# Kernel tuning notes

Measured on AMD Instinct MI355X. Metric: run time of the kernel, lower is better.

## Reference

```python
import jax, jax.numpy as jnp
import numpy as np
from jax import lax

B, S, C_IN, D, H, P, W, DFF, K = 32, 4096, 32, 256, 8, 24, 64, 512, 5
DH = D // H
EPS = 1e-5


def _make_starts():
    stride = max(1, W // 2)
    idx = list(range(0, max(S - W + 1, 1), stride))
    if len(idx) == 0 or idx[-1] != S - W:
        if S - W >= 0:
            idx.append(S - W)
    return np.asarray(idx)

STARTS = _make_starts()                      # [M]
WIDX = STARTS[:, None] + np.arange(W)        # [M, W] patch gather indices


def setup_inputs() -> dict:
    key = jax.random.key(0)
    ks = jax.random.split(key, 24)
    r = lambda i, shape, s=0.02: (jax.random.normal(ks[i], shape, jnp.float32) * s)
    return {
        "x": jax.random.normal(ks[0], (B, S, C_IN), jnp.float32),
        "last_close_unused": jnp.zeros((B,), jnp.float32),
        "dw_w": r(1, (C_IN, 1, K), 0.2),      # depthwise conv kernel
        "pw_w": r(2, (D, C_IN), 0.1),         # pointwise conv (1x1)
        "bn_g": jnp.ones((D,), jnp.float32),
        "bn_b": jnp.zeros((D,), jnp.float32),
        "lg_Wq": r(3, (D, D)), "lg_Wk": r(4, (D, D)),
        "lg_Wv": r(5, (D, D)), "lg_Wo": r(6, (D, D)),
        "dec_Qd": r(7, (P, D), 1.0 / np.sqrt(D)),
        "dec_Wq": r(8, (D, D)), "dec_Wk": r(9, (D, D)),
        "dec_Wv": r(10, (D, D)), "dec_Wo": r(11, (D, D)),
        "ff1_w": r(12, (DFF, D)), "ff1_b": jnp.zeros((DFF,), jnp.float32),
        "ff2_w": r(13, (D, DFF)), "ff2_b": jnp.zeros((D,), jnp.float32),
        "out_w": r(14, (1, D)), "out_b": jnp.zeros((1,), jnp.float32),
        "gate_logits": jnp.tile(jnp.array([0.2, 0.4, 0.4], jnp.float32), (P, 1)),
    }


def _ln(x):
    m = x.mean(-1, keepdims=True)
    v = ((x - m) ** 2).mean(-1, keepdims=True)
    return (x - m) / jnp.sqrt(v + EPS)


def _split(t):  # [B, L, D] -> [B, H, L, DH]
    return t.reshape(t.shape[0], -1, H, DH).transpose(0, 2, 1, 3)


def _mha(Q, KV, Wq, Wk, Wv, scale):
    q = _split(Q @ Wq.T)
    k = _split(KV @ Wk.T)
    v = _split(KV @ Wv.T)
    attn = jax.nn.softmax(jnp.einsum('bhqd,bhkd->bhqk', q, k) * scale, axis=-1)
    o = jnp.einsum('bhqk,bhkd->bhqd', attn, v)
    o = o.transpose(0, 2, 1, 3).reshape(Q.shape[0], -1, D)
    return o, attn


def reference(x, last_close_unused, dw_w, pw_w, bn_g, bn_b,
              lg_Wq, lg_Wk, lg_Wv, lg_Wo,
              dec_Qd, dec_Wq, dec_Wk, dec_Wv, dec_Wo,
              ff1_w, ff1_b, ff2_w, ff2_b, out_w, out_b, gate_logits):
    # --- DepthwisePointwise front-end ---
    xt = jnp.transpose(x, (0, 2, 1))                         # [B, C, S]
    z = lax.conv_general_dilated(xt, dw_w, (1,), [(K // 2, K // 2)],
                                 dimension_numbers=('NCH', 'OIH', 'NCH'),
                                 feature_group_count=C_IN)
    z = jnp.einsum('dc,bcs->bds', pw_w, z)                   # pointwise 1x1
    z = jax.nn.gelu(z, approximate=False)
    m = z.mean((0, 2), keepdims=True)                        # BatchNorm1d (batch stats)
    v = ((z - m) ** 2).mean((0, 2), keepdims=True)
    z = (z - m) / jnp.sqrt(v + EPS) * bn_g[None, :, None] + bn_b[None, :, None]
    z = jnp.transpose(z, (0, 2, 1))                          # [B, S, D]

    # --- LocalGlobalAttention: patch-mean queries over full sequence K/V ---
    Q = z[:, WIDX].mean(axis=2)                              # [B, M, D]
    scale = 1.0 / np.sqrt(DH)
    o, attn_g = _mha(Q, z, lg_Wq, lg_Wk, lg_Wv, scale)
    Hh = _ln(o @ lg_Wo.T + Q)                                # [B, M, D]

    # --- CrossDecoder: learned queries ---
    Qd = jnp.broadcast_to(dec_Qd[None], (B, P, D))
    o2, attn_d = _mha(Qd, Hh, dec_Wq, dec_Wk, dec_Wv, scale)
    z2 = _ln(o2 @ dec_Wo.T + Qd)
    u = jax.nn.gelu(z2 @ ff1_w.T + ff1_b, approximate=False)
    u = _ln(u @ ff2_w.T + ff2_b + z2)
    y_global = (u @ out_w.T + out_b)[..., 0]                 # [B, P]

    # --- Gated combine: residual=0, local=global ---
    g = jax.nn.softmax(gate_logits, axis=-1)                 # [P, 3]
    y = g[:, 1][None, :] * y_global + g[:, 2][None, :] * y_global
    return (y, attn_g, attn_d)
```

## Files before the change

### kernel.cpp

```cpp
#include <hip/hip_runtime.h>
#include <hip/hip_bf16.h>
#include <cmath>

typedef unsigned short u16;
typedef __attribute__((ext_vector_type(4))) float f32x4;
typedef __attribute__((ext_vector_type(8))) short s16x8;

__device__ __forceinline__ float b2f(u16 u) { return __uint_as_float(((unsigned)u) << 16); }
__device__ __forceinline__ u16 f2b(float f) {
    unsigned u = __float_as_uint(f);
    unsigned r = (u + 0x7fffu + ((u >> 16) & 1u)) >> 16;
    return (u16)r;
}
__device__ __forceinline__ float gelu_f(float x) {
    return 0.5f * x * (1.0f + erff(x * 0.70710678118654752f));
}

#define FOLD 0.25503590f

__global__ __launch_bounds__(256) void prep0_k(const float* __restrict__ pw_w,
        const float* __restrict__ lg_Wq, const float* __restrict__ lg_Wo,
        const float* __restrict__ dec_Wk, const float* __restrict__ dec_Wv,
        const float* __restrict__ dec_Wo, const float* __restrict__ ff1_w,
        const float* __restrict__ ff2_w,
        u16* __restrict__ pwb, u16* __restrict__ Wq_b, u16* __restrict__ Wo_b,
        u16* __restrict__ Wk2_b, u16* __restrict__ Wv2_b, u16* __restrict__ Wo2b,
        u16* __restrict__ ff1b, u16* __restrict__ ff2b)
{
    int idx = blockIdx.x * 256 + threadIdx.x;
    if (idx < 327680) {
        int which = idx >> 16, r = idx & 65535;
        const float* srcs[5] = {lg_Wq, lg_Wo, dec_Wk, dec_Wv, dec_Wo};
        u16* dsts[5] = {Wq_b, Wo_b, Wk2_b, Wv2_b, Wo2b};
        dsts[which][r] = f2b(srcs[which][r]);
    } else if (idx < 458752) {
        int r = idx - 327680;
        ff1b[r] = f2b(ff1_w[r]);
    } else if (idx < 589824) {
        int r = idx - 458752;
        ff2b[r] = f2b(ff2_w[r]);
    } else {
        int r = idx - 589824;
        pwb[r] = f2b(pw_w[r]);
    }
}

__global__ __launch_bounds__(256) void dwpw_k(const float* __restrict__ x,
        const float* __restrict__ dw_w, const u16* __restrict__ pwb,
        u16* __restrict__ zp, float* __restrict__ csum, float* __restrict__ csum2)
{
    __shared__ float xs[68][33];
    __shared__ __align__(16) u16 As[64][40];
    const int t = threadIdx.x;
    const int b = blockIdx.x >> 6, s0 = (blockIdx.x & 63) << 6;
    const int r0 = blockIdx.x * 64;
    const int lane = t & 63, w = t >> 6;
    const int l16 = lane & 15, hi = lane >> 4;

    for (int idx = t; idx < 68 * 32; idx += 256) {
        int row = idx >> 5, c = idx & 31;
        int sg = s0 - 2 + row;
        xs[row][c] = (sg >= 0 && sg < 4096) ? x[((size_t)b * 4096 + sg) * 32 + c] : 0.0f;
    }
    const int cc = t & 31;
    float wv[5];
    #pragma unroll
    for (int k = 0; k < 5; ++k) wv[k] = dw_w[cc * 5 + k];
    __syncthreads();
    #pragma unroll
    for (int i = 0; i < 8; ++i) {
        int sl = (t + i * 256) >> 5;
        float acc = 0;
        #pragma unroll
        for (int k = 0; k < 5; ++k) acc += xs[sl + k][cc] * wv[k];
        As[sl][cc] = f2b(acc);
    }
    __syncthreads();

    const int n0 = w * 64;
    f32x4 zero = {0, 0, 0, 0};
    s16x8 bf[4];
    #pragma unroll
    for (int ni = 0; ni < 4; ++ni)
        bf[ni] = *(const s16x8*)(pwb + (n0 + ni * 16 + l16) * 32 + hi * 8);

    float cl[4] = {0,0,0,0}, ch[4] = {0,0,0,0};
    float ql[4] = {0,0,0,0}, qh[4] = {0,0,0,0};

    #pragma unroll
    for (int mi = 0; mi < 4; ++mi) {
        s16x8 af = *(const s16x8*)&As[mi * 16 + l16][hi * 8];
        #pragma unroll
        for (int ni = 0; ni < 4; ++ni) {
            f32x4 acc = __builtin_amdgcn_mfma_f32_16x16x32_bf16(af, bf[ni], zero, 0, 0, 0);
            int col = n0 + ni * 16 + l16;
            int rowb = r0 + mi * 16 + hi * 4;
            #pragma unroll
            for (int r = 0; r < 4; ++r) {
                float e = gelu_f(acc[r]);
                zp[(size_t)(rowb + r) * 256 + col] = f2b(e);
                if (mi < 2) { cl[ni] += e; ql[ni] += e * e; }
                else        { ch[ni] += e; qh[ni] += e * e; }
            }
        }
    }
    #pragma unroll
    for (int ni = 0; ni < 4; ++ni) {
        #pragma unroll
        for (int m = 16; m <= 32; m <<= 1) {
            cl[ni] += __shfl_xor(cl[ni], m);
            ch[ni] += __shfl_xor(ch[ni], m);
            ql[ni] += __shfl_xor(ql[ni], m);
            qh[ni] += __shfl_xor(qh[ni], m);
        }
        if (lane < 16) {
            int col = n0 + ni * 16 + lane;
            size_t bc = (size_t)(r0 >> 5);
            csum [bc * 256 + col]       = cl[ni];
            csum [(bc + 1) * 256 + col] = ch[ni];
            csum2[bc * 256 + col]       = ql[ni];
            csum2[(bc + 1) * 256 + col] = qh[ni];
        }
    }
}

__global__ __launch_bounds__(256) void stats2_k(const float* __restrict__ csum,
        const float* __restrict__ csum2, float* __restrict__ statp)
{
    int j = blockIdx.x, t = threadIdx.x;
    float s1 = 0, s2 = 0;
    for (int i = 0; i < 64; ++i) {
        s1 += csum [(size_t)(j * 64 + i) * 256 + t];
        s2 += csum2[(size_t)(j * 64 + i) * 256 + t];
    }
    statp[j * 512 + t] = s1;
    statp[j * 512 + 256 + t] = s2;
}

__global__ __launch_bounds__(256) void prep1_k(const float* __restrict__ statp,
        const float* __restrict__ bn_g, const float* __restrict__ bn_b,
        const float* __restrict__ gate_logits,
        float* __restrict__ a_ws, float* __restrict__ c_ws, float* __restrict__ coef)
{
    int t = threadIdx.x;
    float s1 = 0, s2 = 0;
    for (int j = 0; j < 64; ++j) {
        s1 += statp[j * 512 + t];
        s2 += statp[j * 512 + 256 + t];
    }
    const float invN = 1.0f / 131072.0f;
    float mean = s1 * invN;
    float var = s2 * invN - mean * mean;
    float av = bn_g[t] * rsqrtf(var + 1e-5f);
    a_ws[t] = av;
    c_ws[t] = bn_b[t] - mean * av;
    if (t < 24) {
        float g0 = gate_logits[t * 3], g1 = gate_logits[t * 3 + 1], g2 = gate_logits[t * 3 + 2];
        float mx = fmaxf(g0, fmaxf(g1, g2));
        float e0 = __expf(g0 - mx), e1 = __expf(g1 - mx), e2 = __expf(g2 - mx);
        coef[t] = (e1 + e2) / (e0 + e1 + e2);
    }
}

__global__ __launch_bounds__(256) void prep2b_k(const float* __restrict__ lg_Wk,
        const float* __restrict__ lg_Wv, const float* __restrict__ a_ws,
        const float* __restrict__ c_ws,
        u16* __restrict__ Wk_b, u16* __restrict__ Wv_b,
        float* __restrict__ betak, float* __restrict__ betav)
{
    __shared__ float red[4];
    int bid = blockIdx.x;
    int which = bid >> 8, row = bid & 255, t = threadIdx.x;
    const float* Wsrc = which ? lg_Wv : lg_Wk;
    float wv = Wsrc[row * 256 + t];
    (which ? Wv_b : Wk_b)[row * 256 + t] = f2b(wv * a_ws[t]);
    float v = wv * c_ws[t];
    for (int m = 32; m; m >>= 1) v += __shfl_xor(v, m);
    if ((t & 63) == 0) red[t >> 6] = v;
    __syncthreads();
    if (t == 0) (which ? betav : betak)[row] = red[0] + red[1] + red[2] + red[3];
}

__global__ __launch_bounds__(256) void q2_k(const float* __restrict__ dec_Qd,
        const float* __restrict__ dec_Wq, float* __restrict__ q2)
{
    __shared__ float wq[16][260];
    __shared__ float qd[24][260];
    int j = blockIdx.x, t = threadIdx.x;
    for (int idx = t; idx < 4096; idx += 256) {
        int tl = idx >> 8, d = idx & 255;
        wq[tl][d] = dec_Wq[(j * 16 + tl) * 256 + d];
    }
    for (int idx = t; idx < 6144; idx += 256) {
        int p = idx >> 8, d = idx & 255;
        qd[p][d] = dec_Qd[idx];
    }
    __syncthreads();
    for (int o = t; o < 384; o += 256) {
        int p = o >> 4, tl = o & 15;
        float s = 0;
        #pragma unroll 8
        for (int d = 0; d < 256; ++d) s += qd[p][d] * wq[tl][d];
        q2[p * 256 + j * 16 + tl] = s;
    }
}

__global__ __launch_bounds__(256) void qgemm_k(const float* __restrict__ csum,
        const float* __restrict__ a_ws, const float* __restrict__ c_ws,
        const u16* __restrict__ W, u16* __restrict__ qb)
{
    __shared__ u16 As[64 * 256];
    __shared__ float aa[256], ccx[256];
    const int t = threadIdx.x;
    const int r0 = blockIdx.x * 64;
    const int lane = t & 63, w = t >> 6;
    const int l16 = lane & 15, hi = lane >> 4;

    aa[t] = a_ws[t] * 0.015625f;
    ccx[t] = c_ws[t];
    __syncthreads();

    #pragma unroll
    for (int i = 0; i < 8; ++i) {
        int c = t + i * 256;
        int row = c >> 5, c16 = c & 31;
        int g = r0 + row, mm = g & 127;
        u16 tmp[8];
        if (mm == 127) {
            #pragma unroll
            for (int j = 0; j < 8; ++j) tmp[j] = 0;
        } else {
            const float* c0p = csum + (size_t)g * 256 + c16 * 8;
            const float* c1p = c0p + 256;
            #pragma unroll
            for (int j = 0; j < 8; ++j) {
                int d = c16 * 8 + j;
                tmp[j] = f2b((c0p[j] + c1p[j]) * aa[d] + ccx[d]);
            }
        }
        int boff = (c16 * 16) ^ ((row & 7) << 4);
        *(s16x8*)((char*)As + row * 512 + boff) = *(s16x8*)tmp;
    }
    __syncthreads();

    const int n0 = w * 64;
    f32x4 zero = {0, 0, 0, 0};
    f32x4 acc[4][4];
    #pragma unroll
    for (int mi = 0; mi < 4; ++mi)
        #pragma unroll
        for (int ni = 0; ni < 4; ++ni) acc[mi][ni] = zero;

    #pragma unroll
    for (int kk = 0; kk < 8; ++kk) {
        s16x8 af[4], bf[4];
        #pragma unroll
        for (int mi = 0; mi < 4; ++mi) {
            int row = mi * 16 + l16;
            int boff = (kk * 64 + hi * 16) ^ ((row & 7) << 4);
            af[mi] = *(const s16x8*)((const char*)As + row * 512 + boff);
        }
        #pragma unroll
        for (int ni = 0; ni < 4; ++ni)
            bf[ni] = *(const s16x8*)(W + (n0 + ni * 16 + l16) * 256 + kk * 32 + hi * 8);
        #pragma unroll
        for (int mi = 0; mi < 4; ++mi)
            #pragma unroll
            for (int ni = 0; ni < 4; ++ni)
                acc[mi][ni] = __builtin_amdgcn_mfma_f32_16x16x32_bf16(af[mi], bf[ni], acc[mi][ni], 0, 0, 0);
    }

    #pragma unroll
    for (int mi = 0; mi < 4; ++mi)
        #pragma unroll
        for (int ni = 0; ni < 4; ++ni) {
            int col = n0 + ni * 16 + l16;
            int rowb = r0 + mi * 16 + hi * 4;
            #pragma unroll
            for (int r = 0; r < 4; ++r)
                qb[(size_t)(rowb + r) * 256 + col] = f2b(acc[mi][ni][r] * FOLD);
        }
}

__global__ __launch_bounds__(256) void kv_k(const u16* __restrict__ zp,
        const u16* __restrict__ Wk, const u16* __restrict__ Wv,
        const float* __restrict__ betak, const float* __restrict__ betav,
        u16* __restrict__ kb, u16* __restrict__ vT)
{
    __shared__ u16 As[64 * 256];
    const int t = threadIdx.x;
    const int r0 = blockIdx.x * 64;
    const int lane = t & 63, w = t >> 6;
    const int l16 = lane & 15, hi = lane >> 4;

    const u16* Ag = zp + (size_t)r0 * 256;
    #pragma unroll
    for (int i = 0; i < 8; ++i) {
        int c = t + i * 256;
        int row = c >> 5, c16 = c & 31;
        s16x8 v = *(const s16x8*)(Ag + row * 256 + c16 * 8);
        int boff = (c16 * 16) ^ ((row & 7) << 4);
        *(s16x8*)((char*)As + row * 512 + boff) = v;
    }
    __syncthreads();

    const int n0 = w * 64;
    f32x4 zero = {0, 0, 0, 0};
    f32x4 acc[4][4];
    #pragma unroll
    for (int mi = 0; mi < 4; ++mi)
        #pragma unroll
        for (int ni = 0; ni < 4; ++ni) acc[mi][ni] = zero;

    #pragma unroll
    for (int kk = 0; kk < 8; ++kk) {
        s16x8 af[4], bfk[4];
        #pragma unroll
        for (int mi = 0; mi < 4; ++mi) {
            int row = mi * 16 + l16;
            int boff = (kk * 64 + hi * 16) ^ ((row & 7) << 4);
            af[mi] = *(const s16x8*)((const char*)As + row * 512 + boff);
        }
        #pragma unroll
        for (int ni = 0; ni < 4; ++ni)
            bfk[ni] = *(const s16x8*)(Wk + (n0 + ni * 16 + l16) * 256 + kk * 32 + hi * 8);
        #pragma unroll
        for (int mi = 0; mi < 4; ++mi)
            #pragma unroll
            for (int ni = 0; ni < 4; ++ni)
                acc[mi][ni] = __builtin_amdgcn_mfma_f32_16x16x32_bf16(af[mi], bfk[ni], acc[mi][ni], 0, 0, 0);
    }
    #pragma unroll
    for (int mi = 0; mi < 4; ++mi)
        #pragma unroll
        for (int ni = 0; ni < 4; ++ni) {
            int col = n0 + ni * 16 + l16;
            float bv = betak[col];
            int rowb = r0 + mi * 16 + hi * 4;
            #pragma unroll
            for (int r = 0; r < 4; ++r)
                kb[(size_t)(rowb + r) * 256 + col] = f2b(acc[mi][ni][r] + bv);
        }

    #pragma unroll
    for (int mi = 0; mi < 4; ++mi)
        #pragma unroll
        for (int ni = 0; ni < 4; ++ni) acc[mi][ni] = zero;
    #pragma unroll
    for (int kk = 0; kk < 8; ++kk) {
        s16x8 af[4], bfv[4];
        #pragma unroll
        for (int mi = 0; mi < 4; ++mi) {
            int row = mi * 16 + l16;
            int boff = (kk * 64 + hi * 16) ^ ((row & 7) << 4);
            af[mi] = *(const s16x8*)((const char*)As + row * 512 + boff);
        }
        #pragma unroll
        for (int ni = 0; ni < 4; ++ni)
            bfv[ni] = *(const s16x8*)(Wv + (n0 + ni * 16 + l16) * 256 + kk * 32 + hi * 8);
        #pragma unroll
        for (int mi = 0; mi < 4; ++mi)
            #pragma unroll
            for (int ni = 0; ni < 4; ++ni)
                acc[mi][ni] = __builtin_amdgcn_mfma_f32_16x16x32_bf16(af[mi], bfv[ni], acc[mi][ni], 0, 0, 0);
    }
    const int b = r0 >> 12, sbase = r0 & 4095;
    #pragma unroll
    for (int mi = 0; mi < 4; ++mi)
        #pragma unroll
        for (int ni = 0; ni < 4; ++ni) {
            int col = n0 + ni * 16 + l16;
            float bv = betav[col];
            int h = col >> 5, dh = col & 31;
            int s = sbase + mi * 16 + hi * 4;
            ushort4 pk;
            pk.x = f2b(acc[mi][ni][0] + bv);
            pk.y = f2b(acc[mi][ni][1] + bv);
            pk.z = f2b(acc[mi][ni][2] + bv);
            pk.w = f2b(acc[mi][ni][3] + bv);
            *(ushort4*)(vT + ((size_t)((b * 8 + h) * 32 + dh)) * 4096 + s) = pk;
        }
}

template<int MODE>
__global__ __launch_bounds__(256) void gemm_g(const u16* __restrict__ A,
        const u16* __restrict__ W, const float* __restrict__ bias,
        void* __restrict__ Cout, int K, int ntn)
{
    __shared__ u16 As[64 * 256];
    const int t = threadIdx.x;
    const int rt = blockIdx.x / ntn, nt = blockIdx.x % ntn;
    const int r0 = rt * 64, N = ntn * 256;
    const int lane = t & 63, w = t >> 6;
    const int l16 = lane & 15, hi = lane >> 4;

    const u16* Ag = A + (size_t)r0 * K;
    const int n0 = w * 64;
    f32x4 zero = {0, 0, 0, 0};
    f32x4 acc[4][4];
    #pragma unroll
    for (int mi = 0; mi < 4; ++mi)
        #pragma unroll
        for (int ni = 0; ni < 4; ++ni) acc[mi][ni] = zero;

    for (int kc = 0; kc < K; kc += 256) {
        if (kc) __syncthreads();
        #pragma unroll
        for (int i = 0; i < 8; ++i) {
            int c = t + i * 256;
            int row = c >> 5, c16 = c & 31;
            s16x8 v = *(const s16x8*)(Ag + (size_t)row * K + kc + c16 * 8);
            int boff = (c16 * 16) ^ ((row & 7) << 4);
            *(s16x8*)((char*)As + row * 512 + boff) = v;
        }
        __syncthreads();
        #pragma unroll
        for (int kk = 0; kk < 8; ++kk) {
            s16x8 af[4], bf[4];
            #pragma unroll
            for (int mi = 0; mi < 4; ++mi) {
                int row = mi * 16 + l16;
                int boff = (kk * 64 + hi * 16) ^ ((row & 7) << 4);
                af[mi] = *(const s16x8*)((const char*)As + row * 512 + boff);
            }
            #pragma unroll
            for (int ni = 0; ni < 4; ++ni) {
                int j = nt * 256 + n0 + ni * 16 + l16;
                bf[ni] = *(const s16x8*)(W + (size_t)j * K + kc + kk * 32 + hi * 8);
            }
            #pragma unroll
            for (int mi = 0; mi < 4; ++mi)
                #pragma unroll
                for (int ni = 0; ni < 4; ++ni)
                    acc[mi][ni] = __builtin_amdgcn_mfma_f32_16x16x32_bf16(af[mi], bf[ni], acc[mi][ni], 0, 0, 0);
        }
    }

    #pragma unroll
    for (int mi = 0; mi < 4; ++mi)
        #pragma unroll
        for (int ni = 0; ni < 4; ++ni) {
            int col = nt * 256 + n0 + ni * 16 + l16;
            float bv = bias ? bias[col] : 0.0f;
            int rowb = r0 + mi * 16 + hi * 4;
            #pragma unroll
            for (int r = 0; r < 4; ++r) {
                float v = acc[mi][ni][r] + bv;
                if (MODE == 0)      ((u16*)Cout)[(size_t)(rowb + r) * N + col] = f2b(v);
                else if (MODE == 1) ((float*)Cout)[(size_t)(rowb + r) * N + col] = v;
                else                ((u16*)Cout)[(size_t)(rowb + r) * N + col] = f2b(gelu_f(v));
            }
        }
}

__global__ __launch_bounds__(256) void gemm_dual(const u16* __restrict__ A,
        const u16* __restrict__ W0, const u16* __restrict__ W1,
        u16* __restrict__ C0, u16* __restrict__ C1)
{
    __shared__ u16 As[64 * 256];
    const int t = threadIdx.x;
    const int which = blockIdx.x >> 6;
    const int r0 = (blockIdx.x & 63) * 64;
    const u16* W = which ? W1 : W0;
    u16* C = which ? C1 : C0;
    const int lane = t & 63, w = t >> 6;
    const int l16 = lane & 15, hi = lane >> 4;

    const u16* Ag = A + (size_t)r0 * 256;
    #pragma unroll
    for (int i = 0; i < 8; ++i) {
        int c = t + i * 256;
        int row = c >> 5, c16 = c & 31;
        s16x8 v = *(const s16x8*)(Ag + row * 256 + c16 * 8);
        int boff = (c16 * 16) ^ ((row & 7) << 4);
        *(s16x8*)((char*)As + row * 512 + boff) = v;
    }
    __syncthreads();

    const int n0 = w * 64;
    f32x4 zero = {0, 0, 0, 0};
    f32x4 acc[4][4];
    #pragma unroll
    for (int mi = 0; mi < 4; ++mi)
        #pragma unroll
        for (int ni = 0; ni < 4; ++ni) acc[mi][ni] = zero;

    #pragma unroll
    for (int kk = 0; kk < 8; ++kk) {
        s16x8 af[4], bf[4];
        #pragma unroll
        for (int mi = 0; mi < 4; ++mi) {
            int row = mi * 16 + l16;
            int boff = (kk * 64 + hi * 16) ^ ((row & 7) << 4);
            af[mi] = *(const s16x8*)((const char*)As + row * 512 + boff);
        }
        #pragma unroll
        for (int ni = 0; ni < 4; ++ni)
            bf[ni] = *(const s16x8*)(W + (n0 + ni * 16 + l16) * 256 + kk * 32 + hi * 8);
        #pragma unroll
        for (int mi = 0; mi < 4; ++mi)
            #pragma unroll
            for (int ni = 0; ni < 4; ++ni)
                acc[mi][ni] = __builtin_amdgcn_mfma_f32_16x16x32_bf16(af[mi], bf[ni], acc[mi][ni], 0, 0, 0);
    }
    #pragma unroll
    for (int mi = 0; mi < 4; ++mi)
        #pragma unroll
        for (int ni = 0; ni < 4; ++ni) {
            int col = n0 + ni * 16 + l16;
            int rowb = r0 + mi * 16 + hi * 4;
            #pragma unroll
            for (int r = 0; r < 4; ++r)
                C[(size_t)(rowb + r) * 256 + col] = f2b(acc[mi][ni][r]);
        }
}

__global__ __launch_bounds__(512) void attn_p1(const u16* __restrict__ qb,
        const u16* __restrict__ kb, const u16* __restrict__ vT,
        float* __restrict__ den, float* __restrict__ o_part)
{
    const int bid = blockIdx.x;
    const int b = bid >> 6, h = (bid >> 3) & 7, chunk = bid & 7;
    const int t = threadIdx.x, w = t >> 6, lane = t & 63;
    const int l16 = lane & 15, hi = lane >> 4;

    __shared__ u16 p_lds[8][16][48];

    s16x8 qf = *(const s16x8*)(qb + ((size_t)(b * 128 + w * 16 + l16)) * 256 + h * 32 + hi * 8);
    const u16* kbase = kb + (size_t)b * 4096 * 256 + h * 32 + hi * 8;
    const u16* vbase = vT + ((size_t)(b * 8 + h)) * 32 * 4096 + hi * 8;

    float dacc[4] = {0, 0, 0, 0};
    f32x4 zero = {0, 0, 0, 0};
    f32x4 oacc[2]; oacc[0] = zero; oacc[1] = zero;

    const int sbeg = chunk * 512, send = sbeg + 512;
    s16x8 kf0 = *(const s16x8*)(kbase + (size_t)(sbeg + l16) * 256);
    s16x8 kf1 = *(const s16x8*)(kbase + (size_t)(sbeg + 16 + l16) * 256);
    s16x8 vf0 = *(const s16x8*)(vbase + ((size_t)l16) * 4096 + sbeg);
    s16x8 vf1 = *(const s16x8*)(vbase + ((size_t)(16 + l16)) * 4096 + sbeg);

    for (int s0 = sbeg; s0 < send; s0 += 32) {
        s16x8 k0 = kf0, k1 = kf1, v0 = vf0, v1 = vf1;
        int sn = s0 + 32;
        if (sn < send) {
            kf0 = *(const s16x8*)(kbase + (size_t)(sn + l16) * 256);
            kf1 = *(const s16x8*)(kbase + (size_t)(sn + 16 + l16) * 256);
            vf0 = *(const s16x8*)(vbase + ((size_t)l16) * 4096 + sn);
            vf1 = *(const s16x8*)(vbase + ((size_t)(16 + l16)) * 4096 + sn);
        }
        f32x4 lg0 = __builtin_amdgcn_mfma_f32_16x16x32_bf16(qf, k0, zero, 0, 0, 0);
        f32x4 lg1 = __builtin_amdgcn_mfma_f32_16x16x32_bf16(qf, k1, zero, 0, 0, 0);
        #pragma unroll
        for (int r = 0; r < 4; ++r) {
            float e0 = exp2f(lg0[r]);
            float e1 = exp2f(lg1[r]);
            dacc[r] += e0 + e1;
            p_lds[w][hi * 4 + r][l16] = f2b(e0);
            p_lds[w][hi * 4 + r][16 + l16] = f2b(e1);
        }
        s16x8 pf = *(const s16x8*)(&p_lds[w][l16][hi * 8]);
        oacc[0] = __builtin_amdgcn_mfma_f32_16x16x32_bf16(pf, v0, oacc[0], 0, 0, 0);
        oacc[1] = __builtin_amdgcn_mfma_f32_16x16x32_bf16(pf, v1, oacc[1], 0, 0, 0);
    }

    #pragma unroll
    for (int m = 1; m <= 8; m <<= 1) {
        #pragma unroll
        for (int r = 0; r < 4; ++r) dacc[r] += __shfl_xor(dacc[r], m);
    }
    if (l16 == 0) {
        #pragma unroll
        for (int r = 0; r < 4; ++r)
            den[(size_t)chunk * 32768 + (b * 8 + h) * 128 + w * 16 + hi * 4 + r] = dacc[r];
    }
    #pragma unroll
    for (int vi = 0; vi < 2; ++vi)
        #pragma unroll
        for (int r = 0; r < 4; ++r) {
            int mg = w * 16 + hi * 4 + r;
            o_part[(size_t)chunk * 1048576 + (size_t)(b * 128 + mg) * 256 + h * 32 + vi * 16 + l16] = oacc[vi][r];
        }
}

__global__ __launch_bounds__(256) void dinv_k(const float* __restrict__ den, float* __restrict__ den_inv)
{
    int i = blockIdx.x * 256 + threadIdx.x;
    float s = 0;
    #pragma unroll
    for (int c = 0; c < 8; ++c) s += den[(size_t)c * 32768 + i];
    den_inv[i] = 1.0f / s;
}

__global__ __launch_bounds__(256) void norm_k(const float* __restrict__ o_part,
        const float* __restrict__ den_inv, u16* __restrict__ ob)
{
    size_t idx = (size_t)blockIdx.x * 256 + threadIdx.x;
    int row = (int)(idx >> 8);
    int col = (int)(idx & 255);
    int b = row >> 7, m = row & 127, h = col >> 5;
    float s = 0;
    #pragma unroll
    for (int c = 0; c < 8; ++c) s += o_part[(size_t)c * 1048576 + idx];
    ob[idx] = f2b(s * den_inv[b * 1024 + h * 128 + m]);
}

__global__ __launch_bounds__(512) void attn_p2(const u16* __restrict__ qb,
        const u16* __restrict__ kb, const float* __restrict__ den_inv,
        float* __restrict__ attn_out)
{
    const int bid = blockIdx.x;
    const int b = bid >> 6, h = (bid >> 3) & 7, chunk = bid & 7;
    const int t = threadIdx.x, w = t >> 6, lane = t & 63;
    const int l16 = lane & 15, hi = lane >> 4;

    __shared__ float buf[8][16][68];

    s16x8 qf = *(const s16x8*)(qb + ((size_t)(b * 128 + w * 16 + l16)) * 256 + h * 32 + hi * 8);
    const u16* kbase = kb + (size_t)b * 4096 * 256 + h * 32 + hi * 8;

    float rinv[4];
    #pragma unroll
    for (int r = 0; r < 4; ++r)
        rinv[r] = den_inv[b * 1024 + h * 128 + w * 16 + hi * 4 + r];

    f32x4 zero = {0, 0, 0, 0};
    float* ab = attn_out + (size_t)(b * 8 + h) * 127 * 4096;
    const int nrow = (w < 7) ? 16 : 15;

    const int sbeg = chunk * 512, send = sbeg + 512;
    for (int s0 = sbeg; s0 < send; s0 += 64) {
        #pragma unroll
        for (int kk = 0; kk < 4; ++kk) {
            int sg = s0 + kk * 16 + l16;
            s16x8 kf = *(const s16x8*)(kbase + (size_t)sg * 256);
            f32x4 lg = __builtin_amdgcn_mfma_f32_16x16x32_bf16(qf, kf, zero, 0, 0, 0);
            #pragma unroll
            for (int r = 0; r < 4; ++r)
                buf[w][hi * 4 + r][kk * 16 + l16] = exp2f(lg[r]) * rinv[r];
        }
        float* dst = ab + (size_t)(w * 16) * 4096 + s0 + lane;
        for (int r = 0; r < nrow; ++r)
            dst[(size_t)r * 4096] = buf[w][r][lane];
    }
}

__global__ __launch_bounds__(256) void ln_hh(const float* __restrict__ og,
        const float* __restrict__ csum, const float* __restrict__ a_ws,
        const float* __restrict__ c_ws, u16* __restrict__ Hb)
{
    __shared__ float red[8];
    int row = blockIdx.x, t = threadIdx.x;
    int mm = row & 127;
    float qv = 0.0f;
    if (mm != 127)
        qv = (csum[(size_t)row * 256 + t] + csum[(size_t)(row + 1) * 256 + t]) *
             (0.015625f * a_ws[t]) + c_ws[t];
    float v = og[(size_t)row * 256 + t] + qv;
    float s = v;
    for (int m = 32; m; m >>= 1) s += __shfl_xor(s, m);
    if ((t & 63) == 0) red[t >> 6] = s;
    __syncthreads();
    float mean = (red[0] + red[1] + red[2] + red[3]) * (1.0f / 256.0f);
    __syncthreads();
    float d = v - mean;
    float q = d * d;
    for (int m = 32; m; m >>= 1) q += __shfl_xor(q, m);
    if ((t & 63) == 0) red[t >> 6] = q;
    __syncthreads();
    float var = (red[0] + red[1] + red[2] + red[3]) * (1.0f / 256.0f);
    Hb[(size_t)row * 256 + t] = f2b(d * rsqrtf(var + 1e-5f));
}

__global__ __launch_bounds__(256) void dec_attn_k(const float* __restrict__ q2,
        const u16* __restrict__ k2b, const u16* __restrict__ v2b,
        float* __restrict__ attn_d, u16* __restrict__ o2b)
{
    __shared__ float qs2[24 * 32];
    __shared__ float ks[128][33];
    __shared__ float vs[128][33];
    __shared__ float lg2[24 * 128];
    __shared__ float sinv[24];
    int bid = blockIdx.x, b = bid >> 3, h = bid & 7;
    int t = threadIdx.x;
    const float scale = 0.17677669529663687f;
    for (int idx = t; idx < 4096; idx += 256) {
        int row = idx >> 5, c = idx & 31;
        ks[row][c] = b2f(k2b[((size_t)(b * 128 + row)) * 256 + h * 32 + c]);
        vs[row][c] = b2f(v2b[((size_t)(b * 128 + row)) * 256 + h * 32 + c]);
    }
    for (int idx = t; idx < 768; idx += 256) {
        int p = idx >> 5, i = idx & 31;
        qs2[idx] = q2[p * 256 + h * 32 + i];
    }
    __syncthreads();
    for (int idx = t; idx < 3048; idx += 256) {
        int p = idx / 127, m = idx - p * 127;
        float s = 0;
        #pragma unroll 8
        for (int i = 0; i < 32; ++i) s += qs2[p * 32 + i] * ks[m][i];
        lg2[p * 128 + m] = __expf(s * scale);
    }
    __syncthreads();
    if (t < 24) {
        float s = 0;
        for (int m = 0; m < 127; ++m) s += lg2[t * 128 + m];
        sinv[t] = 1.0f / s;
    }
    __syncthreads();
    float* ad = attn_d + (size_t)bid * 24 * 127;
    for (int idx = t; idx < 3048; idx += 256) {
        int p = idx / 127, m = idx - p * 127;
        float av = lg2[p * 128 + m] * sinv[p];
        lg2[p * 128 + m] = av;
        ad[idx] = av;
    }
    __syncthreads();
    for (int idx = t; idx < 768; idx += 256) {
        int p = idx >> 5, dh = idx & 31;
        float s = 0;
        for (int m = 0; m < 127; ++m)
            s += lg2[p * 128 + m] * vs[m][dh];
        o2b[((size_t)(b * 24 + p)) * 256 + h * 32 + dh] = f2b(s);
    }
}

__global__ __launch_bounds__(256) void ln3_k(const float* __restrict__ og2,
        const float* __restrict__ dec_Qd, float* __restrict__ z2f, u16* __restrict__ z2b)
{
    __shared__ float red[8];
    int row = blockIdx.x, p = row % 24, t = threadIdx.x;
    float v = og2[(size_t)row * 256 + t] + dec_Qd[p * 256 + t];
    float s = v;
    for (int m = 32; m; m >>= 1) s += __shfl_xor(s, m);
    if ((t & 63) == 0) red[t >> 6] = s;
    __syncthreads();
    float mean = (red[0] + red[1] + red[2] + red[3]) * (1.0f / 256.0f);
    __syncthreads();
    float d = v - mean, q = d * d;
    for (int m = 32; m; m >>= 1) q += __shfl_xor(q, m);
    if ((t & 63) == 0) red[t >> 6] = q;
    __syncthreads();
    float var = (red[0] + red[1] + red[2] + red[3]) * (1.0f / 256.0f);
    float u = d * rsqrtf(var + 1e-5f);
    z2f[(size_t)row * 256 + t] = u;
    z2b[(size_t)row * 256 + t] = f2b(u);
}

__global__ __launch_bounds__(256) void ln5_k(const float* __restrict__ uraw,
        const float* __restrict__ z2f, const float* __restrict__ out_w,
        const float* __restrict__ out_b, const float* __restrict__ coef,
        float* __restrict__ y)
{
    __shared__ float red[8];
    int row = blockIdx.x, p = row % 24, t = threadIdx.x;
    float v = uraw[(size_t)row * 256 + t] + z2f[(size_t)row * 256 + t];
    float s = v;
    for (int m = 32; m; m >>= 1) s += __shfl_xor(s, m);
    if ((t & 63) == 0) red[t >> 6] = s;
    __syncthreads();
    float mean = (red[0] + red[1] + red[2] + red[3]) * (1.0f / 256.0f);
    __syncthreads();
    float d = v - mean, q = d * d;
    for (int m = 32; m; m >>= 1) q += __shfl_xor(q, m);
    if ((t & 63) == 0) red[t >> 6] = q;
    __syncthreads();
    float var = (red[0] + red[1] + red[2] + red[3]) * (1.0f / 256.0f);
    float u = d * rsqrtf(var + 1e-5f);
    __syncthreads();
    float yp = u * out_w[t];
    for (int m = 32; m; m >>= 1) yp += __shfl_xor(yp, m);
    if ((t & 63) == 0) red[t >> 6] = yp;
    __syncthreads();
    if (t == 0) {
        float tot = red[0] + red[1] + red[2] + red[3] + out_b[0];
        y[row] = coef[p] * tot;
    }
}

extern "C" void kernel_launch(void* const* d_in, const int* in_sizes, int n_in,
                              void* d_out, int out_size, void* d_ws, size_t ws_size,
                              hipStream_t stream)
{
    const float* x        = (const float*)d_in[0];
    const float* dw_w     = (const float*)d_in[2];
    const float* pw_w     = (const float*)d_in[3];
    const float* bn_g     = (const float*)d_in[4];
    const float* bn_b     = (const float*)d_in[5];
    const float* lg_Wq    = (const float*)d_in[6];
    const float* lg_Wk    = (const float*)d_in[7];
    const float* lg_Wv    = (const float*)d_in[8];
    const float* lg_Wo    = (const float*)d_in[9];
    const float* dec_Qd   = (const float*)d_in[10];
    const float* dec_Wq   = (const float*)d_in[11];
    const float* dec_Wk   = (const float*)d_in[12];
    const float* dec_Wv   = (const float*)d_in[13];
    const float* dec_Wo   = (const float*)d_in[14];
    const float* ff1_w    = (const float*)d_in[15];
    const float* ff1_b    = (const float*)d_in[16];
    const float* ff2_w    = (const float*)d_in[17];
    const float* ff2_b    = (const float*)d_in[18];
    const float* out_w    = (const float*)d_in[19];
    const float* out_b    = (const float*)d_in[20];
    const float* gate_lg  = (const float*)d_in[21];

    char* ws = (char*)d_ws;
    size_t off = 0;
    auto alloc = [&](size_t bytes) -> void* {
        void* p = ws + off;
        off = (off + bytes + 255) & ~(size_t)255;
        return p;
    };
    u16*   zp    = (u16*)  alloc(67108864);
    u16*   kb    = (u16*)  alloc(67108864);
    u16*   vT    = (u16*)  alloc(67108864);
    float* csum  = (float*)alloc(4194304);
    float* csum2 = (float*)alloc(4194304);
    u16*   qb    = (u16*)  alloc(2097152);
    u16*   ob    = (u16*)  alloc(2097152);
    float* og    = (float*)alloc(4194304);
    u16*   Hb    = (u16*)  alloc(2097152);
    u16*   k2b   = (u16*)  alloc(2097152);
    u16*   v2b   = (u16*)  alloc(2097152);
    float* o_part= (float*)alloc(33554432);
    u16*   o2b   = (u16*)  alloc(393216);
    float* og2   = (float*)alloc(786432);
    float* z2f   = (float*)alloc(786432);
    u16*   z2b   = (u16*)  alloc(393216);
    u16*   u1b   = (u16*)  alloc(786432);
    float* uraw  = (float*)alloc(786432);
    float* q2    = (float*)alloc(24576);
    float* den   = (float*)alloc(1048576);
    float* den_i = (float*)alloc(131072);
    float* statp = (float*)alloc(131072);
    float* a_ws  = (float*)alloc(1024);
    float* c_ws  = (float*)alloc(1024);
    float* betak = (float*)alloc(1024);
    float* betav = (float*)alloc(1024);
    float* coef  = (float*)alloc(256);
    u16*   pwb   = (u16*)  alloc(16384);
    u16*   Wk_b  = (u16*)  alloc(131072);
    u16*   Wv_b  = (u16*)  alloc(131072);
    u16*   Wq_b  = (u16*)  alloc(131072);
    u16*   Wo_b  = (u16*)  alloc(131072);
    u16*   Wk2_b = (u16*)  alloc(131072);
    u16*   Wv2_b = (u16*)  alloc(131072);
    u16*   Wo2b  = (u16*)  alloc(131072);
    u16*   ff1b  = (u16*)  alloc(262144);
    u16*   ff2b  = (u16*)  alloc(262144);

    float* y_out  = (float*)d_out;
    float* attn_g = y_out + 768;
    float* attn_d = attn_g + (size_t)32 * 8 * 127 * 4096;

    prep0_k<<<2336, 256, 0, stream>>>(pw_w, lg_Wq, lg_Wo, dec_Wk, dec_Wv, dec_Wo, ff1_w, ff2_w,
                                      pwb, Wq_b, Wo_b, Wk2_b, Wv2_b, Wo2b, ff1b, ff2b);
    dwpw_k<<<2048, 256, 0, stream>>>(x, dw_w, pwb, zp, csum, csum2);
    stats2_k<<<64, 256, 0, stream>>>(csum, csum2, statp);
    prep1_k<<<1, 256, 0, stream>>>(statp, bn_g, bn_b, gate_lg, a_ws, c_ws, coef);
    prep2b_k<<<512, 256, 0, stream>>>(lg_Wk, lg_Wv, a_ws, c_ws, Wk_b, Wv_b, betak, betav);
    q2_k<<<16, 256, 0, stream>>>(dec_Qd, dec_Wq, q2);
    qgemm_k<<<64, 256, 0, stream>>>(csum, a_ws, c_ws, Wq_b, qb);
    kv_k<<<2048, 256, 0, stream>>>(zp, Wk_b, Wv_b, betak, betav, kb, vT);
    attn_p1<<<2048, 512, 0, stream>>>(qb, kb, vT, den, o_part);
    dinv_k<<<128, 256, 0, stream>>>(den, den_i);
    norm_k<<<4096, 256, 0, stream>>>(o_part, den_i, ob);
    attn_p2<<<2048, 512, 0, stream>>>(qb, kb, den_i, attn_g);
    gemm_g<1><<<64, 256, 0, stream>>>(ob, Wo_b, nullptr, og, 256, 1);
    ln_hh<<<4096, 256, 0, stream>>>(og, csum, a_ws, c_ws, Hb);
    gemm_dual<<<128, 256, 0, stream>>>(Hb, Wk2_b, Wv2_b, k2b, v2b);
    dec_attn_k<<<256, 256, 0, stream>>>(q2, k2b, v2b, attn_d, o2b);
    gemm_g<1><<<12, 256, 0, stream>>>(o2b, Wo2b, nullptr, og2, 256, 1);
    ln3_k<<<768, 256, 0, stream>>>(og2, dec_Qd, z2f, z2b);
    gemm_g<2><<<24, 256, 0, stream>>>(z2b, ff1b, ff1_b, u1b, 256, 2);
    gemm_g<1><<<12, 256, 0, stream>>>(u1b, ff2b, ff2_b, uraw, 512, 1);
    ln5_k<<<768, 256, 0, stream>>>(uraw, z2f, out_w, out_b, coef, y_out);
}
```

Before: 554.6 us.

## Tile V-transpose layout via LDS, vectorize norm and attn stores, tanh GELU

kv_k now stages the V output through a swizzled shared-memory tile and writes 64-position blocks of vT contiguously, which changes the vT layout. attn_p1 indexes vT with the matching blocked addressing. norm_k is vectorized to float4 loads and ushort4 stores with a quarter of the blocks. attn_p2 writes the attention matrix with float4 stores instead of scalar stores. GELU is switched from exact erf to a tanh approximation, which changes numerics slightly away from the exact erf the reference uses.

Result: no change. 563.5 us (+1.6%).

```diff
diff --git a/kernel.cpp b/kernel.cpp
--- a/kernel.cpp
+++ b/kernel.cpp
@@ -13,7 +13,9 @@
     return (u16)r;
 }
 __device__ __forceinline__ float gelu_f(float x) {
-    return 0.5f * x * (1.0f + erff(x * 0.70710678118654752f));
+    float t = x * (0.7978845608f + 0.0356774081f * x * x);
+    float e = exp2f(2.885390082f * t);
+    return 0.5f * x * (1.0f + (e - 1.0f) / (e + 1.0f));
 }
 
 #define FOLD 0.25503590f
@@ -287,7 +289,8 @@
         const float* __restrict__ betak, const float* __restrict__ betav,
         u16* __restrict__ kb, u16* __restrict__ vT)
 {
-    __shared__ u16 As[64 * 256];
+    __shared__ __align__(16) char smem[36864];
+    u16* As = (u16*)smem;
     const int t = threadIdx.x;
     const int r0 = blockIdx.x * 64;
     const int lane = t & 63, w = t >> 6;
@@ -300,7 +303,7 @@
         int row = c >> 5, c16 = c & 31;
         s16x8 v = *(const s16x8*)(Ag + row * 256 + c16 * 8);
         int boff = (c16 * 16) ^ ((row & 7) << 4);
-        *(s16x8*)((char*)As + row * 512 + boff) = v;
+        *(s16x8*)(smem + row * 512 + boff) = v;
     }
     __syncthreads();
 
@@ -319,7 +322,7 @@
         for (int mi = 0; mi < 4; ++mi) {
             int row = mi * 16 + l16;
             int boff = (kk * 64 + hi * 16) ^ ((row & 7) << 4);
-            af[mi] = *(const s16x8*)((const char*)As + row * 512 + boff);
+            af[mi] = *(const s16x8*)(smem + row * 512 + boff);
         }
         #pragma unroll
         for (int ni = 0; ni < 4; ++ni)
@@ -353,7 +356,7 @@
         for (int mi = 0; mi < 4; ++mi) {
             int row = mi * 16 + l16;
             int boff = (kk * 64 + hi * 16) ^ ((row & 7) << 4);
-            af[mi] = *(const s16x8*)((const char*)As + row * 512 + boff);
+            af[mi] = *(const s16x8*)(smem + row * 512 + boff);
         }
         #pragma unroll
         for (int ni = 0; ni < 4; ++ni)
@@ -364,22 +367,35 @@
             for (int ni = 0; ni < 4; ++ni)
                 acc[mi][ni] = __builtin_amdgcn_mfma_f32_16x16x32_bf16(af[mi], bfv[ni], acc[mi][ni], 0, 0, 0);
     }
-    const int b = r0 >> 12, sbase = r0 & 4095;
+    __syncthreads();
     #pragma unroll
     for (int mi = 0; mi < 4; ++mi)
         #pragma unroll
         for (int ni = 0; ni < 4; ++ni) {
             int col = n0 + ni * 16 + l16;
             float bv = betav[col];
-            int h = col >> 5, dh = col & 31;
-            int s = sbase + mi * 16 + hi * 4;
+            int rowb = mi * 16 + hi * 4;
             ushort4 pk;
             pk.x = f2b(acc[mi][ni][0] + bv);
             pk.y = f2b(acc[mi][ni][1] + bv);
             pk.z = f2b(acc[mi][ni][2] + bv);
             pk.w = f2b(acc[mi][ni][3] + bv);
-            *(ushort4*)(vT + ((size_t)((b * 8 + h) * 32 + dh)) * 4096 + s) = pk;
-        }
+            char* p = smem + col * 144 + ((((rowb >> 3) ^ (col & 7)) & 7) << 4) + ((rowb & 7) << 1);
+            *(ushort4*)p = pk;
+        }
+    __syncthreads();
+    const int b = r0 >> 12;
+    const int sblk = (r0 & 4095) >> 6;
+    u16* vout = vT + (size_t)(b * 8) * 131072 + (size_t)sblk * 2048;
+    #pragma unroll
+    for (int j = 0; j < 8; ++j) {
+        int gid = j * 256 + t;
+        int col = gid >> 3, oct = gid & 7;
+        const char* p = smem + col * 144 + (((oct ^ (col & 7)) & 7) << 4);
+        s16x8 v = *(const s16x8*)p;
+        int h = col >> 5, dh = col & 31;
+        *(s16x8*)(vout + (size_t)h * 131072 + dh * 64 + oct * 8) = v;
+    }
 }
 
 template<int MODE>
@@ -528,7 +544,7 @@
 
     s16x8 qf = *(const s16x8*)(qb + ((size_t)(b * 128 + w * 16 + l16)) * 256 + h * 32 + hi * 8);
     const u16* kbase = kb + (size_t)b * 4096 * 256 + h * 32 + hi * 8;
-    const u16* vbase = vT + ((size_t)(b * 8 + h)) * 32 * 4096 + hi * 8;
+    const u16* vbase = vT + (size_t)(b * 8 + h) * 131072 + hi * 8;
 
     float dacc[4] = {0, 0, 0, 0};
     f32x4 zero = {0, 0, 0, 0};
@@ -537,8 +553,8 @@
     const int sbeg = chunk * 512, send = sbeg + 512;
     s16x8 kf0 = *(const s16x8*)(kbase + (size_t)(sbeg + l16) * 256);
     s16x8 kf1 = *(const s16x8*)(kbase + (size_t)(sbeg + 16 + l16) * 256);
-    s16x8 vf0 = *(const s16x8*)(vbase + ((size_t)l16) * 4096 + sbeg);
-    s16x8 vf1 = *(const s16x8*)(vbase + ((size_t)(16 + l16)) * 4096 + sbeg);
+    s16x8 vf0 = *(const s16x8*)(vbase + (sbeg >> 6) * 2048 + l16 * 64 + (sbeg & 63));
+    s16x8 vf1 = *(const s16x8*)(vbase + (sbeg >> 6) * 2048 + (16 + l16) * 64 + (sbeg & 63));
 
     for (int s0 = sbeg; s0 < send; s0 += 32) {
         s16x8 k0 = kf0, k1 = kf1, v0 = vf0, v1 = vf1;
@@ -546,8 +562,8 @@
         if (sn < send) {
             kf0 = *(const s16x8*)(kbase + (size_t)(sn + l16) * 256);
             kf1 = *(const s16x8*)(kbase + (size_t)(sn + 16 + l16) * 256);
-            vf0 = *(const s16x8*)(vbase + ((size_t)l16) * 4096 + sn);
-            vf1 = *(const s16x8*)(vbase + ((size_t)(16 + l16)) * 4096 + sn);
+            vf0 = *(const s16x8*)(vbase + (sn >> 6) * 2048 + l16 * 64 + (sn & 63));
+            vf1 = *(const s16x8*)(vbase + (sn >> 6) * 2048 + (16 + l16) * 64 + (sn & 63));
         }
         f32x4 lg0 = __builtin_amdgcn_mfma_f32_16x16x32_bf16(qf, k0, zero, 0, 0, 0);
         f32x4 lg1 = __builtin_amdgcn_mfma_f32_16x16x32_bf16(qf, k1, zero, 0, 0, 0);
@@ -595,14 +611,21 @@
 __global__ __launch_bounds__(256) void norm_k(const float* __restrict__ o_part,
         const float* __restrict__ den_inv, u16* __restrict__ ob)
 {
-    size_t idx = (size_t)blockIdx.x * 256 + threadIdx.x;
-    int row = (int)(idx >> 8);
-    int col = (int)(idx & 255);
-    int b = row >> 7, m = row & 127, h = col >> 5;
-    float s = 0;
-    #pragma unroll
-    for (int c = 0; c < 8; ++c) s += o_part[(size_t)c * 1048576 + idx];
-    ob[idx] = f2b(s * den_inv[b * 1024 + h * 128 + m]);
+    int idx4 = blockIdx.x * 256 + threadIdx.x;
+    int row = idx4 >> 6;
+    int col4 = (idx4 & 63) * 4;
+    int b = row >> 7, m = row & 127, h = col4 >> 5;
+    float4 s = {0, 0, 0, 0};
+    #pragma unroll
+    for (int c = 0; c < 8; ++c) {
+        float4 v = *(const float4*)(o_part + (size_t)c * 1048576 + (size_t)row * 256 + col4);
+        s.x += v.x; s.y += v.y; s.z += v.z; s.w += v.w;
+    }
+    float rinv = den_inv[b * 1024 + h * 128 + m];
+    ushort4 o;
+    o.x = f2b(s.x * rinv); o.y = f2b(s.y * rinv);
+    o.z = f2b(s.z * rinv); o.w = f2b(s.w * rinv);
+    *(ushort4*)(ob + (size_t)row * 256 + col4) = o;
 }
 
 __global__ __launch_bounds__(512) void attn_p2(const u16* __restrict__ qb,
@@ -626,7 +649,8 @@
 
     f32x4 zero = {0, 0, 0, 0};
     float* ab = attn_out + (size_t)(b * 8 + h) * 127 * 4096;
-    const int nrow = (w < 7) ? 16 : 15;
+    const int srow = lane >> 4;
+    const int scol = (lane & 15) * 4;
 
     const int sbeg = chunk * 512, send = sbeg + 512;
     for (int s0 = sbeg; s0 < send; s0 += 64) {
@@ -639,9 +663,14 @@
             for (int r = 0; r < 4; ++r)
                 buf[w][hi * 4 + r][kk * 16 + l16] = exp2f(lg[r]) * rinv[r];
         }
-        float* dst = ab + (size_t)(w * 16) * 4096 + s0 + lane;
-        for (int r = 0; r < nrow; ++r)
-            dst[(size_t)r * 4096] = buf[w][r][lane];
+        #pragma unroll
+        for (int rb = 0; rb < 4; ++rb) {
+            int row = rb * 4 + srow;
+            int mg = w * 16 + row;
+            float4 v = *(const float4*)&buf[w][row][scol];
+            if (mg < 127)
+                *(float4*)(ab + (size_t)mg * 4096 + s0 + scol) = v;
+        }
     }
 }
 
@@ -864,7 +893,7 @@
     kv_k<<<2048, 256, 0, stream>>>(zp, Wk_b, Wv_b, betak, betav, kb, vT);
     attn_p1<<<2048, 512, 0, stream>>>(qb, kb, vT, den, o_part);
     dinv_k<<<128, 256, 0, stream>>>(den, den_i);
-    norm_k<<<4096, 256, 0, stream>>>(o_part, den_i, ob);
+    norm_k<<<1024, 256, 0, stream>>>(o_part, den_i, ob);
     attn_p2<<<2048, 512, 0, stream>>>(qb, kb, den_i, attn_g);
     gemm_g<1><<<64, 256, 0, stream>>>(ob, Wo_b, nullptr, og, 256, 1);
     ln_hh<<<4096, 256, 0, stream>>>(og, csum, a_ws, c_ws, Hb);
```
